# Performance work log

Measured on AMD Instinct MI355X. Metric: run time of the kernel, lower is better.

## Reference

```python
import jax, jax.numpy as jnp
import numpy as np
import math

B, IN_DIM, HID, OUT_DIM = 8192, 64, 256, 4096
N_STEPS = 20


def logx_and_kl(loga, logb, alpha):
    # logx = log(alpha*a + (1-alpha)*b); kl = KL(x || b)
    logx = jnp.logaddexp(loga + jnp.log(alpha), logb + jnp.log(1.0 - alpha))
    kl = jnp.sum(jnp.exp(logx) * (logx - logb), axis=-1, keepdims=True)
    return logx, kl


def dkl_dalpha(loga, logb, logx):
    a_minus_b = jnp.exp(loga) - jnp.exp(logb)
    return jnp.sum(a_minus_b * (logx - logb + 1.0), axis=-1, keepdims=True)


def findalphafork(loga, logb, k, n_steps=N_STEPS):
    def body(i, carry):
        alpha, bot, top = carry
        logx, kl = logx_and_kl(loga, logb, alpha)
        bot = jnp.where(k >= kl, alpha, bot)
        top = jnp.where(k <= kl, alpha, top)
        d = dkl_dalpha(loga, logb, logx)
        delta = (k - kl) / (d + 1e-12)
        alpha = jnp.clip(alpha + delta,
                         bot * (15.0 / 16.0) + top * (1.0 / 16.0),
                         bot * 0.5 + top * 0.5)
        return alpha, bot, top

    init = (jnp.ones_like(k), jnp.zeros_like(k), jnp.ones_like(k))
    alpha, _, _ = jax.lax.fori_loop(0, n_steps, body, init)
    return alpha


def kl_fixed_mixture(k, loga, logb):
    alpha = findalphafork(loga, logb, k)
    return logx_and_kl(loga, logb, alpha)


def setup_inputs() -> dict:
    key = jax.random.key(0)
    ks = jax.random.split(key, 10)
    x = jax.random.normal(ks[0], (B, IN_DIM), dtype=jnp.float32)
    kl_budget = jax.random.uniform(ks[1], (B, 1), dtype=jnp.float32)
    log_base_dist = jax.nn.log_softmax(
        jax.random.normal(ks[2], (B, OUT_DIM), dtype=jnp.float32), axis=-1)
    W0 = jax.random.normal(ks[3], (HID, IN_DIM + 1), dtype=jnp.float32) * (0.05 / math.sqrt(IN_DIM + 1))
    b0 = jax.random.normal(ks[4], (HID,), dtype=jnp.float32) * 0.01
    W1 = jax.random.normal(ks[5], (HID, HID), dtype=jnp.float32) * (1.0 / math.sqrt(HID))
    b1 = jax.random.normal(ks[6], (HID,), dtype=jnp.float32) * 0.01
    W2 = jax.random.normal(ks[7], (OUT_DIM + 1, HID), dtype=jnp.float32) * 0.01
    b2 = jax.random.normal(ks[8], (OUT_DIM + 1,), dtype=jnp.float32) * 0.01
    return {"x": x, "kl_budget": kl_budget, "log_base_dist": log_base_dist,
            "W0": W0, "b0": b0, "W1": W1, "b1": b1, "W2": W2, "b2": b2,
            "actions_left": 16}


def reference(x, kl_budget, log_base_dist, W0, b0, W1, b1, W2, b2, actions_left):
    h = jnp.concatenate([x, kl_budget], axis=-1)  # [B, IN_DIM+1]
    for i, (W, b) in enumerate(((W0, b0), (W1, b1), (W2, b2))):
        if i != 0:
            h = jnp.tanh(h)
        h = h @ W.T + b
    # n_versions_last_layer == 1 -> selected_x = h
    kl_target = jax.nn.sigmoid(h[:, :1] - math.log(actions_left)) * kl_budget + 1e-6
    loga = h[:, 1:] + log_base_dist
    loga = loga - jnp.max(loga, axis=-1, keepdims=True)
    loga = loga - jax.nn.logsumexp(loga, axis=-1, keepdims=True)
    logx, kl_achieved = kl_fixed_mixture(kl_target, loga, log_base_dist)
    return jax.nn.softmax(logx, axis=-1), jnp.square(kl_achieved - kl_target)
```

## Files before the change

### kernel.cpp

```cpp
#include <hip/hip_runtime.h>
#include <hip/hip_bf16.h>
#include <math.h>

typedef float f32x4 __attribute__((ext_vector_type(4)));
typedef __bf16 bf16x8 __attribute__((ext_vector_type(8)));
typedef _Float16 f16;
typedef _Float16 f16x8 __attribute__((ext_vector_type(8)));
typedef unsigned short ushort;

#define NROWS 8192
#define HID 256
#define NCOL 4096
#define NSTEPS 20

static __device__ inline float bf2f(ushort u) {
    union { unsigned int i; float f; } c; c.i = ((unsigned int)u) << 16; return c.f;
}
static __device__ inline ushort f2bf(float x) {
    __hip_bfloat16 h = __float2bfloat16(x);
    union { __hip_bfloat16 h; ushort u; } c; c.h = h; return c.u;
}
static __device__ inline float fast_tanh(float x) {
    float e = __expf(2.0f * x);
    return 1.0f - 2.0f / (e + 1.0f);
}
static __device__ inline void gload_lds16(const void* g, void* l) {
    __builtin_amdgcn_global_load_lds(
        (const __attribute__((address_space(1))) void*)g,
        (__attribute__((address_space(3))) void*)l, 16, 0, 0);
}

__global__ __launch_bounds__(256) void mlp01_kernel(
    const float* __restrict__ x, const float* __restrict__ klb,
    const float* __restrict__ W0, const float* __restrict__ b0,
    const float* __restrict__ W1, const float* __restrict__ b1,
    const float* __restrict__ W2, const float* __restrict__ b2,
    const int* __restrict__ AL,
    ushort* __restrict__ t_ext, float* __restrict__ kt)
{
    __shared__ float xk[8][66];
    __shared__ float h0[8][HID];
    __shared__ float ktred[8][4];
    const int tid = threadIdx.x;
    const int lane = tid & 63, w = tid >> 6;
    const int r0 = blockIdx.x * 8;

    for (int f = tid; f < 8 * 64; f += 256) {
        int r = f >> 6, k = f & 63;
        xk[r][k] = x[(r0 + r) * 64 + k];
    }
    if (tid < 8) xk[tid][64] = klb[r0 + tid];
    __syncthreads();

    {
        float acc[8];
        float bb = b0[tid];
        #pragma unroll
        for (int r = 0; r < 8; r++) acc[r] = bb;
        for (int k = 0; k < 65; k++) {
            float w0 = W0[tid * 65 + k];
            #pragma unroll
            for (int r = 0; r < 8; r++) acc[r] += w0 * xk[r][k];
        }
        #pragma unroll
        for (int r = 0; r < 8; r++) h0[r][tid] = fast_tanh(acc[r]);
    }
    __syncthreads();
    {
        float acc[8];
        float bb = b1[tid];
        #pragma unroll
        for (int r = 0; r < 8; r++) acc[r] = bb;
        for (int k = 0; k < HID; k++) {
            float w1 = W1[tid * HID + k];
            #pragma unroll
            for (int r = 0; r < 8; r++) acc[r] += w1 * h0[r][k];
        }
        const float w2v = W2[tid];
        __syncthreads();
        #pragma unroll
        for (int r = 0; r < 8; r++) {
            float v = fast_tanh(acc[r]);
            ushort hi = f2bf(v);
            float lo = v - bf2f(hi);
            size_t base = (size_t)(r0 + r) * 512;
            t_ext[base + tid] = hi;
            t_ext[base + 256 + tid] = f2bf(lo);
            float p = v * w2v;
            #pragma unroll
            for (int off = 1; off < 64; off <<= 1) p += __shfl_xor(p, off);
            if (lane == 0) ktred[r][w] = p;
        }
        __syncthreads();
        if (tid < 8) {
            float accv = ktred[tid][0] + ktred[tid][1] + ktred[tid][2] + ktred[tid][3];
            float z = accv + b2[0] - logf((float)AL[0]);
            float sg = 1.0f / (1.0f + expf(-z));
            kt[r0 + tid] = sg * klb[r0 + tid] + 1e-6f;
        }
    }
}

__global__ __launch_bounds__(256) void w2ext_kernel(const float* __restrict__ W2,
                                                    const float* __restrict__ b2,
                                                    ushort* __restrict__ Bext,
                                                    float* __restrict__ b2s)
{
    const int r = blockIdx.x, t = threadIdx.x;
    float v = W2[(size_t)(r + 1) * 256 + t];
    ushort hi = f2bf(v);
    float lo = v - bf2f(hi);
    Bext[(size_t)r * 512 + t] = hi;
    Bext[(size_t)r * 512 + 256 + t] = f2bf(lo);
    if (t == 0) b2s[r] = b2[r + 1];
}

__global__ __launch_bounds__(256) void gemm2_mfma(
    const ushort* __restrict__ Aext, const ushort* __restrict__ Bext,
    const float* __restrict__ b2s, f16* __restrict__ h2f)
{
    __shared__ ushort As[128 * 64];
    __shared__ ushort Bs[128 * 64];
    const int tid = threadIdx.x;
    const int lane = tid & 63, w = tid >> 6;
    const int m0 = blockIdx.y * 128, c0 = blockIdx.x * 128;
    const int wm = w & 1, wn = w >> 1;

    f32x4 acc[4][4];
    #pragma unroll
    for (int i = 0; i < 4; i++)
        #pragma unroll
        for (int j = 0; j < 4; j++) acc[i][j] = (f32x4){0.f, 0.f, 0.f, 0.f};

    int sg_row[4], sg_c[4];
    #pragma unroll
    for (int s = 0; s < 4; s++) {
        int idx = (s * 4 + w) * 512 + lane * 8;
        int row = idx >> 6;
        int cp = (idx >> 3) & 7;
        sg_row[s] = row;
        sg_c[s] = cp ^ (row & 7);
    }

    for (int kt = 0; kt < 8; kt++) {
        const int k0 = kt * 64;
        #pragma unroll
        for (int s = 0; s < 4; s++) {
            gload_lds16(&Aext[(size_t)(m0 + sg_row[s]) * 512 + k0 + sg_c[s] * 8],
                        &As[(s * 4 + w) * 512]);
            gload_lds16(&Bext[(size_t)(c0 + sg_row[s]) * 512 + k0 + sg_c[s] * 8],
                        &Bs[(s * 4 + w) * 512]);
        }
        __syncthreads();
        #pragma unroll
        for (int kk = 0; kk < 2; kk++) {
            const int cA = kk * 4 + (lane >> 4);
            bf16x8 af[4], bfr[4];
            #pragma unroll
            for (int i = 0; i < 4; i++) {
                int mr = wm * 64 + i * 16 + (lane & 15);
                af[i] = *(const bf16x8*)&As[mr * 64 + ((cA ^ (mr & 7)) * 8)];
                int nr = wn * 64 + i * 16 + (lane & 15);
                bfr[i] = *(const bf16x8*)&Bs[nr * 64 + ((cA ^ (nr & 7)) * 8)];
            }
            #pragma unroll
            for (int i = 0; i < 4; i++)
                #pragma unroll
                for (int j = 0; j < 4; j++)
                    acc[i][j] = __builtin_amdgcn_mfma_f32_16x16x32_bf16(
                        af[i], bfr[j], acc[i][j], 0, 0, 0);
        }
        __syncthreads();
    }

    const int colb = c0 + wn * 64 + (lane & 15);
    #pragma unroll
    for (int j = 0; j < 4; j++) {
        float bias = b2s[colb + j * 16];
        #pragma unroll
        for (int i = 0; i < 4; i++) {
            int rr = m0 + wm * 64 + i * 16 + (lane >> 4) * 4;
            #pragma unroll
            for (int q = 0; q < 4; q++)
                h2f[(size_t)(rr + q) * 4096 + colb + j * 16] = (f16)(acc[i][j][q] + bias);
        }
    }
}

__global__ __launch_bounds__(512) void solve512(
    float* __restrict__ out, const f16* __restrict__ h2f,
    const float* __restrict__ logb, const float* __restrict__ ktarr)
{
    __shared__ float red[32];
    const int tid = threadIdx.x;
    const int lane = tid & 63, w = tid >> 6;
    const int r = blockIdx.x;

    const f16* hrow = h2f + (size_t)r * 4096;
    const float* brow = logb + (size_t)r * 4096;

    f16x8 h8 = *(const f16x8*)&hrow[tid * 8];
    f32x4 bq0 = *(const f32x4*)&brow[tid * 8];
    f32x4 bq1 = *(const f32x4*)&brow[tid * 8 + 4];

    float av[8], bv[8], e[8];
    float s = 0.0f, sav = 0.0f;
    #pragma unroll
    for (int j = 0; j < 8; j++) {
        av[j] = (float)h8[j];
        bv[j] = (j < 4) ? bq0[j & 3] : bq1[j & 3];
        e[j] = __expf(av[j] + bv[j]);
        s += e[j];
        sav = fmaf(e[j], av[j], sav);
    }
    #pragma unroll
    for (int off = 1; off < 64; off <<= 1) {
        s   += __shfl_xor(s, off);
        sav += __shfl_xor(sav, off);
    }
    if (lane == 0) { red[w * 2] = s; red[w * 2 + 1] = sav; }
    __syncthreads();
    s = 0.0f; sav = 0.0f;
    #pragma unroll
    for (int i = 0; i < 8; i++) { s += red[i * 2]; sav += red[i * 2 + 1]; }

    const float k = ktarr[r];
    const float lns = __logf(s);
    const float inv = 1.0f / s;
    const float kl1 = fmaf(sav, inv, -lns);

    float* orow = out + (size_t)r * 4096;

    if (k >= kl1) {
        f32x4 o0, o1;
        #pragma unroll
        for (int j = 0; j < 4; j++) { o0[j] = e[j] * inv; o1[j] = e[j + 4] * inv; }
        *(f32x4*)&orow[tid * 8] = o0;
        *(f32x4*)&orow[tid * 8 + 4] = o1;
        if (tid == 0) {
            float d = kl1 - k;
            out[(size_t)NROWS * NCOL + r] = d * d;
        }
        return;
    }

    float am[8], eb[8];
    float c2 = 0.0f, c3 = 0.0f, seb = 0.0f, samv = 0.0f;
    #pragma unroll
    for (int j = 0; j < 8; j++) {
        float b = __expf(bv[j]);
        eb[j] = b;
        float a = fmaf(e[j], inv, -b);
        am[j] = a;
        c2   = fmaf(b, bv[j], c2);
        c3   = fmaf(a, bv[j], c3);
        seb += b;
        samv = fmaf(a, av[j], samv);
    }
    #pragma unroll
    for (int off = 1; off < 64; off <<= 1) {
        c2   += __shfl_xor(c2, off);
        c3   += __shfl_xor(c3, off);
        seb  += __shfl_xor(seb, off);
        samv += __shfl_xor(samv, off);
    }
    __syncthreads();
    if (lane == 0) {
        red[w * 4 + 0] = c2;  red[w * 4 + 1] = c3;
        red[w * 4 + 2] = seb; red[w * 4 + 3] = samv;
    }
    __syncthreads();
    c2 = 0.0f; c3 = 0.0f; seb = 0.0f; samv = 0.0f;
    #pragma unroll
    for (int i = 0; i < 8; i++) {
        c2   += red[i * 4 + 0];
        c3   += red[i * 4 + 1];
        seb  += red[i * 4 + 2];
        samv += red[i * 4 + 3];
    }

    const float C2 = c2;
    const float C3 = c3;
    const float C4 = (1.0f - seb) - C3;

    float skl = kl1, a_eval = 1.0f;
    float bot = 0.0f, top = 1.0f;
    float d1 = samv - lns * (1.0f - seb) + (1.0f - seb);
    float alpha = fminf(0.5f, fmaxf(1.0f / 16.0f,
                        1.0f + (k - kl1) / (d1 + 1e-12f)));

    for (int it = 1; it < NSTEPS; it++) {
        a_eval = alpha;
        float kacc = 0.0f, dacc = 0.0f;
        #pragma unroll
        for (int j = 0; j < 8; j++) {
            float xv = fmaf(alpha, am[j], eb[j]);
            float lx = __logf(xv);
            kacc = fmaf(xv, lx, kacc);
            dacc = fmaf(am[j], lx, dacc);
        }
        #pragma unroll
        for (int off = 1; off < 64; off <<= 1) {
            kacc += __shfl_xor(kacc, off);
            dacc += __shfl_xor(dacc, off);
        }
        __syncthreads();
        if (lane == 0) { red[w * 2 + 0] = kacc; red[w * 2 + 1] = dacc; }
        __syncthreads();
        kacc = 0.0f; dacc = 0.0f;
        #pragma unroll
        for (int i = 0; i < 8; i++) { kacc += red[i * 2]; dacc += red[i * 2 + 1]; }

        float klc = kacc - C2 - alpha * C3;
        float dc  = dacc + C4;
        skl = klc;

        bot = (k >= klc) ? alpha : bot;
        top = (k <= klc) ? alpha : top;
        float delta = (k - klc) / (dc + 1e-12f);
        float lo = bot * (15.0f / 16.0f) + top * (1.0f / 16.0f);
        float hi = 0.5f * (bot + top);
        alpha = fminf(hi, fmaxf(lo, alpha + delta));
        if (top - bot < 1e-6f) break;
    }

    if (alpha != a_eval) {
        float kacc = 0.0f;
        #pragma unroll
        for (int j = 0; j < 8; j++) {
            float xv = fmaf(alpha, am[j], eb[j]);
            kacc = fmaf(xv, __logf(xv), kacc);
        }
        #pragma unroll
        for (int off = 1; off < 64; off <<= 1) kacc += __shfl_xor(kacc, off);
        __syncthreads();
        if (lane == 0) red[w] = kacc;
        __syncthreads();
        kacc = 0.0f;
        #pragma unroll
        for (int i = 0; i < 8; i++) kacc += red[i];
        skl = kacc - C2 - alpha * C3;
    }

    const float spx = fmaf(alpha, 1.0f - seb, seb);
    const float invs = 1.0f / spx;
    f32x4 o0, o1;
    #pragma unroll
    for (int j = 0; j < 4; j++) {
        o0[j] = fmaf(alpha, am[j], eb[j]) * invs;
        o1[j] = fmaf(alpha, am[j + 4], eb[j + 4]) * invs;
    }
    *(f32x4*)&orow[tid * 8] = o0;
    *(f32x4*)&orow[tid * 8 + 4] = o1;
    if (tid == 0) {
        float d = skl - k;
        out[(size_t)NROWS * NCOL + r] = d * d;
    }
}

extern "C" void kernel_launch(void* const* d_in, const int* in_sizes, int n_in,
                              void* d_out, int out_size, void* d_ws, size_t ws_size,
                              hipStream_t stream)
{
    const float* x    = (const float*)d_in[0];
    const float* klb  = (const float*)d_in[1];
    const float* logb = (const float*)d_in[2];
    const float* W0   = (const float*)d_in[3];
    const float* b0   = (const float*)d_in[4];
    const float* W1   = (const float*)d_in[5];
    const float* b1   = (const float*)d_in[6];
    const float* W2   = (const float*)d_in[7];
    const float* b2   = (const float*)d_in[8];
    const int*   AL   = (const int*)d_in[9];
    float* out = (float*)d_out;

    const size_t MB = 1048576ull;
    char* p = (char*)d_ws;
    ushort* tws  = (ushort*)(p);
    ushort* Bext = (ushort*)(p + 8 * MB);
    float*  kt   = (float*) (p + 12 * MB);
    float*  b2s  = (float*) (p + 12 * MB + 65536);
    f16*    h2f  = (f16*)   (p + 16 * MB);

    hipLaunchKernelGGL(mlp01_kernel, dim3(1024), dim3(256), 0, stream,
                       x, klb, W0, b0, W1, b1, W2, b2, AL, tws, kt);
    hipLaunchKernelGGL(w2ext_kernel, dim3(4096), dim3(256), 0, stream, W2, b2, Bext, b2s);
    hipLaunchKernelGGL(gemm2_mfma, dim3(32, 64), dim3(256), 0, stream, tws, Bext, b2s, h2f);
    hipLaunchKernelGGL(solve512, dim3(8192), dim3(512), 0, stream, out, h2f, logb, kt);
}
```

Baseline: 172.8 us.

## Transpose MLP weights in prep kernel and process 16 rows per block

Adds a prep kernel that transposes W0 and W1 and also absorbs the W2 split work, so that in the MLP kernel each thread reads weights coalesced across threads rather than with a large stride. The MLP kernel now handles 16 rows per block instead of 8, halving the grid and reusing each weight load across more rows. The cost is an extra global transpose write and read plus higher register and LDS use per block, with fewer blocks available to fill the GPU.

```diff
diff --git a/kernel.cpp b/kernel.cpp
--- a/kernel.cpp
+++ b/kernel.cpp
@@ -30,56 +30,73 @@
         (__attribute__((address_space(3))) void*)l, 16, 0, 0);
 }
 
+__global__ __launch_bounds__(256) void prep_kernel(
+    const float* __restrict__ W2, const float* __restrict__ b2,
+    const float* __restrict__ W0, const float* __restrict__ W1,
+    ushort* __restrict__ Bext, float* __restrict__ b2s,
+    float* __restrict__ W0t, float* __restrict__ W1t)
+{
+    const int r = blockIdx.x, t = threadIdx.x;
+    float v = W2[(size_t)(r + 1) * 256 + t];
+    ushort hi = f2bf(v);
+    float lo = v - bf2f(hi);
+    Bext[(size_t)r * 512 + t] = hi;
+    Bext[(size_t)r * 512 + 256 + t] = f2bf(lo);
+    if (t == 0) b2s[r] = b2[r + 1];
+    if (r < 256) W1t[r * 256 + t] = W1[t * 256 + r];
+    if (r < 65)  W0t[r * 256 + t] = W0[t * 65 + r];
+}
+
 __global__ __launch_bounds__(256) void mlp01_kernel(
     const float* __restrict__ x, const float* __restrict__ klb,
-    const float* __restrict__ W0, const float* __restrict__ b0,
-    const float* __restrict__ W1, const float* __restrict__ b1,
+    const float* __restrict__ W0t, const float* __restrict__ b0,
+    const float* __restrict__ W1t, const float* __restrict__ b1,
     const float* __restrict__ W2, const float* __restrict__ b2,
     const int* __restrict__ AL,
     ushort* __restrict__ t_ext, float* __restrict__ kt)
 {
-    __shared__ float xk[8][66];
-    __shared__ float h0[8][HID];
-    __shared__ float ktred[8][4];
+    __shared__ float xk[16][66];
+    __shared__ float h0[16][HID];
+    __shared__ float ktred[16][4];
     const int tid = threadIdx.x;
     const int lane = tid & 63, w = tid >> 6;
-    const int r0 = blockIdx.x * 8;
-
-    for (int f = tid; f < 8 * 64; f += 256) {
+    const int r0 = blockIdx.x * 16;
+
+    for (int f = tid; f < 16 * 64; f += 256) {
         int r = f >> 6, k = f & 63;
-        xk[r][k] = x[(r0 + r) * 64 + k];
-    }
-    if (tid < 8) xk[tid][64] = klb[r0 + tid];
+        xk[r][k] = x[(size_t)(r0 + r) * 64 + k];
+    }
+    if (tid < 16) xk[tid][64] = klb[r0 + tid];
     __syncthreads();
 
     {
-        float acc[8];
+        float acc[16];
         float bb = b0[tid];
         #pragma unroll
-        for (int r = 0; r < 8; r++) acc[r] = bb;
+        for (int r = 0; r < 16; r++) acc[r] = bb;
         for (int k = 0; k < 65; k++) {
-            float w0 = W0[tid * 65 + k];
-            #pragma unroll
-            for (int r = 0; r < 8; r++) acc[r] += w0 * xk[r][k];
-        }
-        #pragma unroll
-        for (int r = 0; r < 8; r++) h0[r][tid] = fast_tanh(acc[r]);
+            float wv = W0t[k * 256 + tid];
+            #pragma unroll
+            for (int r = 0; r < 16; r++) acc[r] = fmaf(wv, xk[r][k], acc[r]);
+        }
+        #pragma unroll
+        for (int r = 0; r < 16; r++) h0[r][tid] = fast_tanh(acc[r]);
     }
     __syncthreads();
     {
-        float acc[8];
+        float acc[16];
         float bb = b1[tid];
         #pragma unroll
-        for (int r = 0; r < 8; r++) acc[r] = bb;
+        for (int r = 0; r < 16; r++) acc[r] = bb;
         for (int k = 0; k < HID; k++) {
-            float w1 = W1[tid * HID + k];
-            #pragma unroll
-            for (int r = 0; r < 8; r++) acc[r] += w1 * h0[r][k];
+            float wv = W1t[k * 256 + tid];
+            #pragma unroll
+            for (int r = 0; r < 16; r++) acc[r] = fmaf(wv, h0[r][k], acc[r]);
         }
         const float w2v = W2[tid];
         __syncthreads();
         #pragma unroll
-        for (int r = 0; r < 8; r++) {
+        for (int r = 0; r < 16; r++) {
             float v = fast_tanh(acc[r]);
             ushort hi = f2bf(v);
             float lo = v - bf2f(hi);
@@ -92,27 +109,13 @@
             if (lane == 0) ktred[r][w] = p;
         }
         __syncthreads();
-        if (tid < 8) {
+        if (tid < 16) {
             float accv = ktred[tid][0] + ktred[tid][1] + ktred[tid][2] + ktred[tid][3];
             float z = accv + b2[0] - logf((float)AL[0]);
             float sg = 1.0f / (1.0f + expf(-z));
             kt[r0 + tid] = sg * klb[r0 + tid] + 1e-6f;
         }
     }
-}
-
-__global__ __launch_bounds__(256) void w2ext_kernel(const float* __restrict__ W2,
-                                                    const float* __restrict__ b2,
-                                                    ushort* __restrict__ Bext,
-                                                    float* __restrict__ b2s)
-{
-    const int r = blockIdx.x, t = threadIdx.x;
-    float v = W2[(size_t)(r + 1) * 256 + t];
-    ushort hi = f2bf(v);
-    float lo = v - bf2f(hi);
-    Bext[(size_t)r * 512 + t] = hi;
-    Bext[(size_t)r * 512 + 256 + t] = f2bf(lo);
-    if (t == 0) b2s[r] = b2[r + 1];
 }
 
 __global__ __launch_bounds__(256) void gemm2_mfma(
@@ -375,16 +378,20 @@
     float* out = (float*)d_out;
 
     const size_t MB = 1048576ull;
+    const size_t KB = 1024ull;
     char* p = (char*)d_ws;
     ushort* tws  = (ushort*)(p);
     ushort* Bext = (ushort*)(p + 8 * MB);
     float*  kt   = (float*) (p + 12 * MB);
-    float*  b2s  = (float*) (p + 12 * MB + 65536);
+    float*  b2s  = (float*) (p + 12 * MB + 64 * KB);
+    float*  W0t  = (float*) (p + 12 * MB + 128 * KB);
+    float*  W1t  = (float*) (p + 12 * MB + 256 * KB);
     f16*    h2f  = (f16*)   (p + 16 * MB);
 
-    hipLaunchKernelGGL(mlp01_kernel, dim3(1024), dim3(256), 0, stream,
-                       x, klb, W0, b0, W1, b1, W2, b2, AL, tws, kt);
-    hipLaunchKernelGGL(w2ext_kernel, dim3(4096), dim3(256), 0, stream, W2, b2, Bext, b2s);
+    hipLaunchKernelGGL(prep_kernel, dim3(4096), dim3(256), 0, stream,
+                       W2, b2, W0, W1, Bext, b2s, W0t, W1t);
+    hipLaunchKernelGGL(mlp01_kernel, dim3(512), dim3(256), 0, stream,
+                       x, klb, W0t, b0, W1t, b1, W2, b2, AL, tws, kt);
     hipLaunchKernelGGL(gemm2_mfma, dim3(32, 64), dim3(256), 0, stream, tws, Bext, b2s, h2f);
     hipLaunchKernelGGL(solve512, dim3(8192), dim3(512), 0, stream, out, h2f, logb, kt);
 }
```

After: 172.0 us. No clear change (-0.5%).
